# Performance work log

Measured on AMD Instinct MI355X. Metric: run time of the kernel, lower is better.

## Reference

```python
import jax, jax.numpy as jnp
import numpy as np
from jax import lax

H = 256       # hidden_size (hard-coded via .view(256,1) in source)
V = 10000     # vocab
NOPS = 9      # ops: 0 sum, 1 count, 2 diff, 3 greater, 4 lesser, 5 and, 6 or, 7 assign, 8 reset
COLS = 64
ROWS = 200000
T = 4         # num_time_steps
QLEN = 40
NNUM = 5


def setup_inputs() -> dict:
    key = jax.random.key(0)
    ks = jax.random.split(key, 16)
    s = 0.02
    return {
        'input_question': jax.random.randint(ks[0], (QLEN,), 0, V),
        'question_numbers': jax.random.normal(ks[1], (NNUM,), jnp.float32),
        'left_word_indices': jax.random.randint(ks[2], (NNUM,), 0, QLEN),
        'table': jax.random.normal(ks[3], (ROWS, COLS), jnp.float32),
        # question RNN params
        'E': jax.random.normal(ks[4], (V, H), jnp.float32) * s,
        'Wx': jax.random.normal(ks[5], (H, H), jnp.float32) * s,
        'Wh': jax.random.normal(ks[6], (H, H), jnp.float32) * s,
        'b': jnp.zeros((H,), jnp.float32),
        # selector params
        'W_op': jax.random.normal(ks[7], (H, 2 * H), jnp.float32) * s,
        'op_emb': jax.random.normal(ks[8], (NOPS, H), jnp.float32) * s,
        'W_col': jax.random.normal(ks[9], (H, 2 * H), jnp.float32) * s,
        'col_emb': jax.random.normal(ks[10], (COLS, H), jnp.float32) * s,
        # pivot embeddings U(0)=lesser, U(1)=greater
        'U': jax.random.normal(ks[11], (2, H), jnp.float32) * s,
        # history RNN params
        'W_hc': jax.random.normal(ks[12], (H, 2 * H), jnp.float32) * s,
        'W_hh': jax.random.normal(ks[13], (H, H), jnp.float32) * s,
    }


def reference(input_question, question_numbers, left_word_indices, table,
              E, Wx, Wh, b, W_op, op_emb, W_col, col_emb, U, W_hc, W_hh):
    rows = table.shape[0]
    # ---- question RNN (simple tanh RNN over embedded words) ----
    x = E[input_question]                                  # [Q, H]
    def cell(h, xt):
        hn = jnp.tanh(xt @ Wx + h @ Wh + b)
        return hn, hn
    q, states = lax.scan(cell, jnp.zeros((H,), table.dtype), x)   # q: [H], states: [Q, H]
    Z = states[left_word_indices]                          # z_matrix [N, H]

    # ---- pivots (train mode: soft attention over question numbers) ----
    beta_l = jax.nn.softmax(Z @ U[0])                      # [N]
    beta_g = jax.nn.softmax(Z @ U[1])
    l_pivot = beta_l @ question_numbers                    # scalar
    g_pivot = beta_g @ question_numbers

    row_selects = [jnp.ones((rows,), table.dtype)]
    scalars = [jnp.zeros((), table.dtype)]
    h_hist = jnp.zeros((H,), table.dtype)
    lookup = jnp.zeros(table.shape, table.dtype)

    for t in range(T):
        qh = jnp.concatenate([q, h_hist])                  # [2H]
        a_op = jax.nn.softmax(op_emb @ jnp.tanh(W_op @ qh))    # [NOPS]
        a_col = jax.nn.softmax(col_emb @ jnp.tanh(W_col @ qh)) # [COLS]

        rs1 = row_selects[-1]
        rs2 = row_selects[max(0, len(row_selects) - 2)]
        s1 = scalars[-1]
        s3 = scalars[max(0, len(scalars) - 3)]

        col_val = table @ a_col                            # [R] column-weighted table values
        g_sel = (table > g_pivot).astype(table.dtype) @ a_col  # [R]
        l_sel = (table < l_pivot).astype(table.dtype) @ a_col

        row_select = (a_op[3] * g_sel + a_op[4] * l_sel
                      + a_op[5] * jnp.minimum(rs1, rs2)
                      + a_op[6] * jnp.maximum(rs1, rs2)
                      + a_op[8] * 1.0
                      + (a_op[0] + a_op[1] + a_op[2] + a_op[7]) * rs1)

        scalar = (a_op[0] * (rs1 @ col_val)
                  + a_op[1] * jnp.sum(rs1)
                  + a_op[2] * (s3 - s1))

        lookup = a_op[7] * row_select[:, None] * a_col[None, :]   # [R, C]

        c = jnp.concatenate([a_op @ op_emb, a_col @ col_emb])     # [2H]
        h_hist = jnp.tanh(W_hc @ c + W_hh @ h_hist)

        row_selects.append(row_select)
        scalars.append(scalar)

    return scalars[-1], lookup
```

## Files before the change

kernel.cpp:

```cpp
#include <hip/hip_runtime.h>
#include <hip/hip_fp16.h>
#include <math.h>

#define H 256
#define COLSN 64
#define ROWSN 200000
#define T_STEPS 4
#define QLEN 40
#define NNUM 5
#define NOPS 9

#define WS_XWB    0
#define WS_Q      10240
#define WS_AOP    10496
#define WS_ACOL   10560
#define WS_PIV    10816
#define WS_TICKET 10818
#define WS_PACC8  10824
#define WS_MOP    11104
#define WS_MCOL   13408
#define WS_WPK    30720
#define WS_END    (30720 + 768*128 + 512*128)

#define NTBL_TILES  1563
#define NTBL_BLOCKS 782
#define NXW 10
#define NMB 72
#define NPK 20

template<int CTRL>
__device__ __forceinline__ float dpp_add(float x) {
    int xi = __float_as_int(x);
    int yi = __builtin_amdgcn_update_dpp(0, xi, CTRL, 0xF, 0xF, true);
    return x + __int_as_float(yi);
}
#define DPP_XOR1 0xB1
#define DPP_XOR2 0x4E
#define DPP_HMIR 0x141
#define DPP_MIR  0x140

__device__ __forceinline__ float reduce16(float v) {
    v = dpp_add<DPP_XOR1>(v);
    v = dpp_add<DPP_XOR2>(v);
    v = dpp_add<DPP_HMIR>(v);
    v = dpp_add<DPP_MIR>(v);
    return v;
}

__device__ __forceinline__ float fast_tanh(float x) {
    float cx = fminf(15.f, fmaxf(-15.f, x));
    float e = __expf(2.f * cx);
    return __fdividef(e - 1.f, e + 1.f);
}

__device__ __forceinline__ float dot4(float4 a, float4 b) {
    return a.x * b.x + a.y * b.y + a.z * b.z + a.w * b.w;
}

__device__ __forceinline__ int sw(int i) { return i + ((i >> 4) << 2); }

__device__ __forceinline__ const float* wrow_src(int o,
        const float* W_op, const float* W_col, const float* W_hh) {
    if (o < 256)  return &W_op[(long)o * 512 + 256];
    if (o < 512)  return &W_col[(long)(o - 256) * 512 + 256];
    if (o < 768)  return &W_hh[(long)(o - 512) * 256];
    if (o < 1024) return &W_op[(long)(o - 768) * 512];
    return &W_col[(long)(o - 1024) * 512];
}

__global__ __launch_bounds__(1024) void k_pre(const int* __restrict__ iq,
        const float* __restrict__ E, const float* __restrict__ Wx,
        const float* __restrict__ b, const float* __restrict__ W_hc,
        const float* __restrict__ op_emb, const float* __restrict__ col_emb,
        const float* __restrict__ W_op, const float* __restrict__ W_col,
        const float* __restrict__ W_hh, float* __restrict__ ws) {
    int blk = blockIdx.x;
    int tid = threadIdx.x;
    if (blk < NXW) {
        if (blk == 0 && tid < 16) ws[WS_TICKET + tid] = 0.f;
        int widx = blk * 4 + (tid >> 8);
        int i = tid & 255;
        int word = iq[widx];
        const float* erow = E + (long)word * H;
        float a0 = b[i], a1 = 0.f, a2 = 0.f, a3 = 0.f;
        #pragma unroll 8
        for (int j = 0; j < H; j += 4) {
            a0 += erow[j + 0] * Wx[(j + 0) * H + i];
            a1 += erow[j + 1] * Wx[(j + 1) * H + i];
            a2 += erow[j + 2] * Wx[(j + 2) * H + i];
            a3 += erow[j + 3] * Wx[(j + 3) * H + i];
        }
        ws[WS_XWB + widx * H + i] = (a0 + a1) + (a2 + a3);
    } else if (blk < NXW + NMB) {
        __shared__ __attribute__((aligned(16))) float tile[32][268];
        int mb = blk - NXW;
        int bi = mb / 9;
        int kg = mb % 9;
        int ibase = bi * 32;
        int coff = (kg == 0) ? 0 : H;
        for (int idx = tid; idx < 32 * 64; idx += 1024) {
            int rr = idx >> 6, c4 = idx & 63;
            float4 v = *(const float4*)&W_hc[(long)(ibase + rr) * 512 + coff + c4 * 4];
            float* d = &tile[rr][c4 * 4];
            d[0] = v.x; d[1] = v.y; d[2] = v.z; d[3] = v.w;
        }
        __syncthreads();
        int io = tid >> 5;
        int l32 = tid & 31;
        int nk = (kg == 0) ? NOPS : 8;
        for (int kk = 0; kk < nk; ++kk) {
            const float* emb;
            int dst;
            if (kg == 0) { emb = op_emb + kk * H; dst = WS_MOP + kk * H; }
            else { int c = (kg - 1) * 8 + kk; emb = col_emb + c * H; dst = WS_MCOL + c * H; }
            float s = 0.f;
            #pragma unroll
            for (int q8 = 0; q8 < 8; ++q8) {
                int q = (q8 + l32) & 7;
                s += tile[io][l32 * 8 + q] * emb[l32 * 8 + q];
            }
            s += __shfl_xor(s, 1);
            s += __shfl_xor(s, 2);
            s += __shfl_xor(s, 4);
            s += __shfl_xor(s, 8);
            s += __shfl_xor(s, 16);
            if (l32 == 0) ws[dst + ibase + io] = s;
        }
    } else {
        int pb2 = blk - NXW - NMB;
        int wb = pb2 * 64;
        __half2* wpk = (__half2*)(ws + WS_WPK);
        for (int idx = tid; idx < 64 * 128; idx += 1024) {
            int rr = idx >> 7, j2 = idx & 127;
            int o = wb + rr;
            const float* src = wrow_src(o, W_op, W_col, W_hh);
            float2 v = *(const float2*)&src[j2 * 2];
            wpk[(long)o * 128 + j2] = __floats2half2_rn(v.x, v.y);
        }
    }
}

__global__ __launch_bounds__(1024) void k_rnn(const float* __restrict__ Wh,
                      const int* __restrict__ lwi,
                      const float* __restrict__ U, const float* __restrict__ qn,
                      float* __restrict__ ws) {
    __shared__ __attribute__((aligned(16))) float hbuf[2][288];
    __shared__ __attribute__((aligned(16))) float xwb[QLEN][H];
    __shared__ float Z[NNUM][H];
    __shared__ float lg[10];
    int tid = threadIdx.x;
    int g = tid >> 3;
    int p = tid & 7;

    float2 w2[32];
    #pragma unroll
    for (int jj = 0; jj < 32; ++jj)
        w2[jj] = *(const float2*)&Wh[(p * 32 + jj) * H + g * 2];

    {
        const float4* src = (const float4*)&ws[WS_XWB];
        float4* dst = (float4*)&xwb[0][0];
        for (int idx = tid; idx < QLEN * H / 4; idx += 1024) dst[idx] = src[idx];
    }
    if (tid < H) hbuf[0][tid + ((tid >> 5) << 2)] = 0.f;
    __syncthreads();

    int lw0 = lwi[0], lw1 = lwi[1], lw2 = lwi[2], lw3 = lwi[3], lw4 = lwi[4];
    int cur = 0;
    for (int t = 0; t < QLEN; ++t) {
        const float4* hv = (const float4*)&hbuf[cur][p * 36];
        float a0 = 0.f, a1 = 0.f;
        #pragma unroll
        for (int q4 = 0; q4 < 8; ++q4) {
            float4 h4 = hv[q4];
            float2 wa = w2[q4 * 4 + 0];
            float2 wb = w2[q4 * 4 + 1];
            float2 wc = w2[q4 * 4 + 2];
            float2 wd = w2[q4 * 4 + 3];
            a0 += h4.x * wa.x; a1 += h4.x * wa.y;
            a0 += h4.y * wb.x; a1 += h4.y * wb.y;
            a0 += h4.z * wc.x; a1 += h4.z * wc.y;
            a0 += h4.w * wd.x; a1 += h4.w * wd.y;
        }
        a0 = dpp_add<DPP_XOR1>(a0); a0 = dpp_add<DPP_XOR2>(a0); a0 = dpp_add<DPP_HMIR>(a0);
        a1 = dpp_add<DPP_XOR1>(a1); a1 = dpp_add<DPP_XOR2>(a1); a1 = dpp_add<DPP_HMIR>(a1);
        if (p < 2) {
            float s = (p == 0) ? a0 : a1;
            int i = g * 2 + p;
            float hn = fast_tanh(xwb[t][i] + s);
            hbuf[cur ^ 1][i + ((i >> 5) << 2)] = hn;
            if (t == lw0) Z[0][i] = hn;
            if (t == lw1) Z[1][i] = hn;
            if (t == lw2) Z[2][i] = hn;
            if (t == lw3) Z[3][i] = hn;
            if (t == lw4) Z[4][i] = hn;
        }
        __syncthreads();
        cur ^= 1;
    }
    if (tid < H) ws[WS_Q + tid] = hbuf[cur][tid + ((tid >> 5) << 2)];

    int grp = tid >> 5;
    int lane = tid & 31;
    if (grp < 10) {
        int u = grp / 5, n = grp % 5;
        float s = 0.f;
        #pragma unroll
        for (int k = 0; k < 8; ++k) {
            int j = lane + k * 32;
            s += Z[n][j] * U[u * H + j];
        }
        s += __shfl_xor(s, 1);
        s += __shfl_xor(s, 2);
        s += __shfl_xor(s, 4);
        s += __shfl_xor(s, 8);
        s += __shfl_xor(s, 16);
        if (lane == 0) lg[grp] = s;
    }
    __syncthreads();
    if (tid < 2) {
        float m = -1e30f;
        for (int n = 0; n < 5; ++n) m = fmaxf(m, lg[tid * 5 + n]);
        float e[5], s = 0.f;
        for (int n = 0; n < 5; ++n) { e[n] = expf(lg[tid * 5 + n] - m); s += e[n]; }
        float piv = 0.f;
        for (int n = 0; n < 5; ++n) piv += (e[n] / s) * qn[n];
        ws[WS_PIV + (tid == 0 ? 1 : 0)] = piv;
    }
}

template<bool PACKED>
__device__ __forceinline__ void sel_body(
        const float* __restrict__ W_op, const float* __restrict__ W_col,
        const float* __restrict__ W_hh, const float* __restrict__ op_emb,
        const float* __restrict__ col_emb, float* __restrict__ ws) {
    __shared__ float mlds[73 * 256];
    __shared__ __attribute__((aligned(16))) float hl[320];
    __shared__ __attribute__((aligned(16))) float uop[320];
    __shared__ __attribute__((aligned(16))) float ucol[320];
    __shared__ float vhh[256];
    __shared__ float Pl[512];
    __shared__ float lgs[80];
    __shared__ float aop_s[16], acol_s[64];
    const int tid = threadIdx.x;
    const int r  = tid >> 4;
    const int p  = tid & 15;
    const int pb = p * 20;
    const __half2* wpk = (const __half2*)(ws + WS_WPK);

    for (int idx = tid; idx < 73 * 256; idx += 1024) mlds[idx] = ws[WS_MOP + idx];
    if (tid < 256) hl[sw(tid)] = ws[WS_Q + tid];
    __syncthreads();

    {
        float4 q0 = *(const float4*)&hl[pb + 0];
        float4 q1 = *(const float4*)&hl[pb + 4];
        float4 q2 = *(const float4*)&hl[pb + 8];
        float4 q3 = *(const float4*)&hl[pb + 12];
        float qv[16] = {q0.x,q0.y,q0.z,q0.w, q1.x,q1.y,q1.z,q1.w,
                        q2.x,q2.y,q2.z,q2.w, q3.x,q3.y,q3.z,q3.w};
        #pragma unroll 2
        for (int m = 0; m < 8; ++m) {
            int o = m * 64 + r;
            float s = 0.f;
            if (PACKED) {
                const __half2* row = wpk + (long)(768 + o) * 128 + p * 8;
                #pragma unroll
                for (int jj = 0; jj < 8; ++jj) {
                    float2 w = __half22float2(row[jj]);
                    s += w.x * qv[2 * jj] + w.y * qv[2 * jj + 1];
                }
            } else {
                const float* row = (o < 256) ? &W_op[(long)o * 512 + p * 16]
                                             : &W_col[(long)(o - 256) * 512 + p * 16];
                s = dot4(*(const float4*)&row[0], q0) + dot4(*(const float4*)&row[4], q1)
                  + dot4(*(const float4*)&row[8], q2) + dot4(*(const float4*)&row[12], q3);
            }
            s = reduce16(s);
            if (p == 0) Pl[o] = s;
        }
    }
    __syncthreads();
    if (tid < 256) {
        uop[sw(tid)]  = fast_tanh(Pl[tid]);
        ucol[sw(tid)] = fast_tanh(Pl[256 + tid]);
        vhh[tid] = 0.f;
    }
    __syncthreads();

    for (int t = 0; t < T_STEPS; ++t) {
        {
            const float* urow = &ucol[pb];
            float4 u0 = *(const float4*)&urow[0];
            float4 u1 = *(const float4*)&urow[4];
            float4 u2 = *(const float4*)&urow[8];
            float4 u3 = *(const float4*)&urow[12];
            const float* erow = &col_emb[r * 256 + p * 16];
            float s = dot4(*(const float4*)&erow[0], u0) + dot4(*(const float4*)&erow[4], u1)
                    + dot4(*(const float4*)&erow[8], u2) + dot4(*(const float4*)&erow[12], u3);
            s = reduce16(s);
            if (p == 0) lgs[NOPS + r] = s;
            if (r < NOPS) {
                const float* vrow = &uop[pb];
                float4 v0 = *(const float4*)&vrow[0];
                float4 v1 = *(const float4*)&vrow[4];
                float4 v2 = *(const float4*)&vrow[8];
                float4 v3 = *(const float4*)&vrow[12];
                const float* orow = &op_emb[r * 256 + p * 16];
                float so = dot4(*(const float4*)&orow[0], v0) + dot4(*(const float4*)&orow[4], v1)
                         + dot4(*(const float4*)&orow[8], v2) + dot4(*(const float4*)&orow[12], v3);
                so = reduce16(so);
                if (p == 0) lgs[r] = so;
            }
        }
        __syncthreads();
        if (tid == 0) {
            float m = -1e30f;
            for (int k = 0; k < NOPS; ++k) m = fmaxf(m, lgs[k]);
            float e[NOPS], s = 0.f;
            for (int k = 0; k < NOPS; ++k) { e[k] = expf(lgs[k] - m); s += e[k]; }
            float inv = 1.f / s;
            for (int k = 0; k < NOPS; ++k) {
                float a = e[k] * inv;
                aop_s[k] = a;
                ws[WS_AOP + t * 16 + k] = a;
            }
        }
        if (tid >= 64 && tid < 128) {
            int lane = tid - 64;
            float v = lgs[NOPS + lane];
            float m = v;
            for (int off = 1; off < 64; off <<= 1) m = fmaxf(m, __shfl_xor(m, off));
            float e = expf(v - m);
            float s = e;
            for (int off = 1; off < 64; off <<= 1) s += __shfl_xor(s, off);
            float a = __fdividef(e, s);
            acol_s[lane] = a;
            ws[WS_ACOL + t * COLSN + lane] = a;
        }
        __syncthreads();
        if (t < T_STEPS - 1) {
            if (tid < 256) {
                float s = vhh[tid];
                #pragma unroll
                for (int k = 0; k < NOPS; ++k) s += aop_s[k] * mlds[k * 256 + tid];
                #pragma unroll 8
                for (int c = 0; c < COLSN; ++c) s += acol_s[c] * mlds[(NOPS + c) * 256 + tid];
                hl[sw(tid)] = fast_tanh(s);
            }
            __syncthreads();
            {
                float4 h0 = *(const float4*)&hl[pb + 0];
                float4 h1 = *(const float4*)&hl[pb + 4];
                float4 h2 = *(const float4*)&hl[pb + 8];
                float4 h3 = *(const float4*)&hl[pb + 12];
                float hv2[16] = {h0.x,h0.y,h0.z,h0.w, h1.x,h1.y,h1.z,h1.w,
                                 h2.x,h2.y,h2.z,h2.w, h3.x,h3.y,h3.z,h3.w};
                #pragma unroll 2
                for (int m = 0; m < 12; ++m) {
                    int o = m * 64 + r;
                    float s = 0.f;
                    if (PACKED) {
                        const __half2* row = wpk + (long)o * 128 + p * 8;
                        #pragma unroll
                        for (int jj = 0; jj < 8; ++jj) {
                            float2 w = __half22float2(row[jj]);
                            s += w.x * hv2[2 * jj] + w.y * hv2[2 * jj + 1];
                        }
                    } else {
                        const float* row;
                        if (o < 256)      row = &W_op[(long)o * 512 + 256 + p * 16];
                        else if (o < 512) row = &W_col[(long)(o - 256) * 512 + 256 + p * 16];
                        else              row = &W_hh[(long)(o - 512) * 256 + p * 16];
                        s = dot4(*(const float4*)&row[0], h0) + dot4(*(const float4*)&row[4], h1)
                          + dot4(*(const float4*)&row[8], h2) + dot4(*(const float4*)&row[12], h3);
                    }
                    s = reduce16(s);
                    if (p == 0) {
                        if (o < 256)      uop[sw(o)] = fast_tanh(Pl[o] + s);
                        else if (o < 512) ucol[sw(o - 256)] = fast_tanh(Pl[o] + s);
                        else              vhh[o - 512] = s;
                    }
                }
            }
            __syncthreads();
        }
    }
}

__global__ __launch_bounds__(1024) void k_sel2_f16(
        const float* __restrict__ W_op, const float* __restrict__ W_col,
        const float* __restrict__ W_hh, const float* __restrict__ op_emb,
        const float* __restrict__ col_emb, float* __restrict__ ws) {
    sel_body<true>(W_op, W_col, W_hh, op_emb, col_emb, ws);
}
__global__ __launch_bounds__(1024) void k_sel2_f32(
        const float* __restrict__ W_op, const float* __restrict__ W_col,
        const float* __restrict__ W_hh, const float* __restrict__ op_emb,
        const float* __restrict__ col_emb, float* __restrict__ ws) {
    sel_body<false>(W_op, W_col, W_hh, op_emb, col_emb, ws);
}

__global__ __launch_bounds__(512) void k_table(const float* __restrict__ table,
                                               float* __restrict__ ws,
                                               float* __restrict__ out) {
    __shared__ __attribute__((aligned(16))) float4 acT4[4][17];
    __shared__ float aop_l[64];
    __shared__ float rs3s[8][16];
    __shared__ float bred[8][8];
    __shared__ int lastblk;
    const int tid = threadIdx.x;
    const int wid = tid >> 6;
    const int lane = tid & 63;
    const int r16 = lane & 15;
    const int q = lane >> 4;

    if (tid < 64) {
        aop_l[tid] = ws[WS_AOP + tid];
        acT4[tid >> 4][tid & 15] = make_float4(
            ws[WS_ACOL + 0 * COLSN + tid], ws[WS_ACOL + 1 * COLSN + tid],
            ws[WS_ACOL + 2 * COLSN + tid], ws[WS_ACOL + 3 * COLSN + tid]);
    }
    __syncthreads();
    const float gp = ws[WS_PIV + 0];
    const float lp = ws[WS_PIV + 1];
    const float ac3 = acT4[q][r16].w;

    long wrow0 = (long)blockIdx.x * 128 + wid * 16;
    long wrow1 = (long)(blockIdx.x + NTBL_BLOCKS) * 128 + wid * 16;
    bool act0 = wrow0 < ROWSN;
    bool act1 = wrow1 < ROWSN;

    float4 xa0, xa1, xa2, xa3, xb0, xb1, xb2, xb3;
    if (act0) {
        const float* src = table + (wrow0 + r16) * COLSN + q * 16;
        xa0 = *(const float4*)&src[0];
        xa1 = *(const float4*)&src[4];
        xa2 = *(const float4*)&src[8];
        xa3 = *(const float4*)&src[12];
    }
    if (act1) {
        const float* src = table + (wrow1 + r16) * COLSN + q * 16;
        xb0 = *(const float4*)&src[0];
        xb1 = *(const float4*)&src[4];
        xb2 = *(const float4*)&src[8];
        xb3 = *(const float4*)&src[12];
    }

    float dacc[4] = {0,0,0,0}, cacc[4] = {0,0,0,0};

    #define TBL_TILE(X0, X1, X2, X3, WROW, ACT)                                   \
    {                                                                             \
        float cv[4] = {0,0,0,0}, gs[4] = {0,0,0,0}, ls[4] = {0,0,0,0};            \
        if (ACT) {                                                                \
            float xs[16] = {X0.x,X0.y,X0.z,X0.w, X1.x,X1.y,X1.z,X1.w,             \
                            X2.x,X2.y,X2.z,X2.w, X3.x,X3.y,X3.z,X3.w};            \
            _Pragma("unroll")                                                     \
            for (int jj = 0; jj < 16; ++jj) {                                     \
                float x = xs[jj];                                                 \
                float4 a4 = acT4[q][jj];                                          \
                float gt = (x > gp) ? 1.f : 0.f;                                  \
                float lt = (x < lp) ? 1.f : 0.f;                                  \
                cv[0] += x * a4.x;  cv[1] += x * a4.y;                            \
                cv[2] += x * a4.z;  cv[3] += x * a4.w;                            \
                gs[0] += gt * a4.x; gs[1] += gt * a4.y;                           \
                gs[2] += gt * a4.z; gs[3] += gt * a4.w;                           \
                ls[0] += lt * a4.x; ls[1] += lt * a4.y;                           \
                ls[2] += lt * a4.z; ls[3] += lt * a4.w;                           \
            }                                                                     \
        }                                                                         \
        _Pragma("unroll")                                                         \
        for (int k = 0; k < 4; ++k) {                                             \
            cv[k] += __shfl_xor(cv[k], 16); cv[k] += __shfl_xor(cv[k], 32);       \
            gs[k] += __shfl_xor(gs[k], 16); gs[k] += __shfl_xor(gs[k], 32);       \
            ls[k] += __shfl_xor(ls[k], 16); ls[k] += __shfl_xor(ls[k], 32);       \
        }                                                                         \
        float prev1 = 1.f, prev2 = 1.f;                                           \
        _Pragma("unroll")                                                         \
        for (int t = 0; t < 4; ++t) {                                             \
            if (ACT) { dacc[t] += prev1 * cv[t]; cacc[t] += prev1; }              \
            float cg = aop_l[t*16+3], cl = aop_l[t*16+4], cmn = aop_l[t*16+5];    \
            float cmx = aop_l[t*16+6], co = aop_l[t*16+8];                        \
            float cid = aop_l[t*16+0] + aop_l[t*16+1]                             \
                      + aop_l[t*16+2] + aop_l[t*16+7];                            \
            float rsn = cg * gs[t] + cl * ls[t] + cmn * fminf(prev1, prev2)       \
                      + cmx * fmaxf(prev1, prev2) + co + cid * prev1;             \
            prev2 = prev1; prev1 = rsn;                                           \
        }                                                                         \
        if (q == 0 && ACT) rs3s[wid][r16] = prev1 * aop_l[3*16+7];                \
                        \
        if (ACT) {                                                                \
            float* dst = out + 1 + WROW * COLSN;                                  \
            _Pragma("unroll 4")                                                   \
            for (int s = 0; s < 16; ++s)                                          \
                __builtin_nontemporal_store(rs3s[wid][s] * ac3,                   \
                                            &dst[(long)s * COLSN + lane]);        \
        }                                                                         \
    }

    TBL_TILE(xa0, xa1, xa2, xa3, wrow0, act0)
    TBL_TILE(xb0, xb1, xb2, xb3, wrow1, act1)
    #undef TBL_TILE

    float vals[8];
    #pragma unroll
    for (int t = 0; t < 4; ++t) { vals[t] = dacc[t]; vals[4 + t] = cacc[t]; }
    #pragma unroll
    for (int k = 0; k < 8; ++k) vals[k] = reduce16(vals[k]);
    if (lane == 0) {
        #pragma unroll
        for (int k = 0; k < 8; ++k) bred[wid][k] = vals[k];
    }
    __syncthreads();
    if (tid < 8) {
        float s = 0.f;
        #pragma unroll
        for (int w = 0; w < 8; ++w) s += bred[w][tid];
        atomicAdd(&ws[WS_PACC8 + tid], s);
    }
    __syncthreads();

    if (tid == 0) {
        float old = atomicAdd(&ws[WS_TICKET], 1.0f);
        lastblk = ((int)(old + 0.5f) == NTBL_BLOCKS - 1) ? 1 : 0;
    }
    __syncthreads();
    if (lastblk) {
        if (tid < 8) bred[0][tid] = atomicAdd(&ws[WS_PACC8 + tid], 0.f);
        __syncthreads();
        if (tid == 0) {
            float d0 = bred[0][0], d1 = bred[0][1], d2 = bred[0][2], d3 = bred[0][3];
            float c0 = bred[0][4], c1 = bred[0][5], c2 = bred[0][6], c3 = bred[0][7];
            float s0 = aop_l[0]*d0  + aop_l[1]*c0;
            float s1 = aop_l[16]*d1 + aop_l[17]*c1 + aop_l[18]*(0.f - s0);
            float s2 = aop_l[32]*d2 + aop_l[33]*c2 + aop_l[34]*(0.f - s1);
            float s3 = aop_l[48]*d3 + aop_l[49]*c3 + aop_l[50]*(s0 - s2);
            out[0] = s3;
        }
    }
}

extern "C" void kernel_launch(void* const* d_in, const int* in_sizes, int n_in,
                              void* d_out, int out_size, void* d_ws, size_t ws_size,
                              hipStream_t stream) {
    const int*   iq      = (const int*)  d_in[0];
    const float* qn      = (const float*)d_in[1];
    const int*   lwi     = (const int*)  d_in[2];
    const float* table   = (const float*)d_in[3];
    const float* E       = (const float*)d_in[4];
    const float* Wx      = (const float*)d_in[5];
    const float* Wh      = (const float*)d_in[6];
    const float* b       = (const float*)d_in[7];
    const float* W_op    = (const float*)d_in[8];
    const float* op_emb  = (const float*)d_in[9];
    const float* W_col   = (const float*)d_in[10];
    const float* col_emb = (const float*)d_in[11];
    const float* U       = (const float*)d_in[12];
    const float* W_hc    = (const float*)d_in[13];
    const float* W_hh    = (const float*)d_in[14];
    float* out = (float*)d_out;
    float* ws  = (float*)d_ws;

    const bool packed = ws_size >= (size_t)WS_END * sizeof(float);
    int npre = NXW + NMB + (packed ? NPK : 0);

    hipLaunchKernelGGL(k_pre,  dim3(npre), dim3(1024), 0, stream,
                       iq, E, Wx, b, W_hc, op_emb, col_emb, W_op, W_col, W_hh, ws);
    hipLaunchKernelGGL(k_rnn,  dim3(1), dim3(1024), 0, stream, Wh, lwi, U, qn, ws);
    if (packed)
        hipLaunchKernelGGL(k_sel2_f16, dim3(1), dim3(1024), 0, stream,
                           W_op, W_col, W_hh, op_emb, col_emb, ws);
    else
        hipLaunchKernelGGL(k_sel2_f32, dim3(1), dim3(1024), 0, stream,
                           W_op, W_col, W_hh, op_emb, col_emb, ws);
    hipLaunchKernelGGL(k_table, dim3(NTBL_BLOCKS), dim3(512), 0, stream,
                       table, ws, out);
}
```

Before: 132.1 us.

## Prefetch table into cache with idle blocks during serial RNN and selector kernels

Launches the single-block RNN and selector kernels with 255 extra blocks that stream the whole 51 MB table and discard the values. The aim is to pull the table into the MI355X's on-chip cache (last-level cache) while the serial recurrent work runs, so the bandwidth-bound table kernel reads more of it from cache. The risk is that 51 MB may exceed the cache, and the extra blocks compete with the serial block for resources and bandwidth. The table is also read twice more from HBM in total.

```diff
diff --git a/kernel.cpp b/kernel.cpp
--- a/kernel.cpp
+++ b/kernel.cpp
@@ -27,6 +27,7 @@
 #define NXW 10
 #define NMB 72
 #define NPK 20
+#define NPF 255
 
 template<int CTRL>
 __device__ __forceinline__ float dpp_add(float x) {
@@ -58,6 +59,18 @@
 }
 
 __device__ __forceinline__ int sw(int i) { return i + ((i >> 4) << 2); }
+
+__device__ __forceinline__ void prefetch_table(const float* __restrict__ table,
+                                               int pfid, int tid) {
+    const float4* t4 = (const float4*)table;
+    const long n4 = (long)ROWSN * COLSN / 4;
+    float acc = 0.f;
+    for (long i = (long)pfid * 1024 + tid; i < n4; i += (long)NPF * 1024) {
+        float4 v = t4[i];
+        acc += v.x + v.y + v.z + v.w;
+    }
+    asm volatile("" :: "v"(acc));
+}
 
 __device__ __forceinline__ const float* wrow_src(int o,
         const float* W_op, const float* W_col, const float* W_hh) {
@@ -143,7 +156,11 @@
 __global__ __launch_bounds__(1024) void k_rnn(const float* __restrict__ Wh,
                       const int* __restrict__ lwi,
                       const float* __restrict__ U, const float* __restrict__ qn,
-                      float* __restrict__ ws) {
+                      const float* __restrict__ table, float* __restrict__ ws) {
+    if (blockIdx.x > 0) {
+        prefetch_table(table, blockIdx.x - 1, threadIdx.x);
+        return;
+    }
     __shared__ __attribute__((aligned(16))) float hbuf[2][288];
     __shared__ __attribute__((aligned(16))) float xwb[QLEN][H];
     __shared__ float Z[NNUM][H];
@@ -391,13 +408,17 @@
 __global__ __launch_bounds__(1024) void k_sel2_f16(
         const float* __restrict__ W_op, const float* __restrict__ W_col,
         const float* __restrict__ W_hh, const float* __restrict__ op_emb,
-        const float* __restrict__ col_emb, float* __restrict__ ws) {
+        const float* __restrict__ col_emb, const float* __restrict__ table,
+        float* __restrict__ ws) {
+    if (blockIdx.x > 0) { prefetch_table(table, blockIdx.x - 1, threadIdx.x); return; }
     sel_body<true>(W_op, W_col, W_hh, op_emb, col_emb, ws);
 }
 __global__ __launch_bounds__(1024) void k_sel2_f32(
         const float* __restrict__ W_op, const float* __restrict__ W_col,
         const float* __restrict__ W_hh, const float* __restrict__ op_emb,
-        const float* __restrict__ col_emb, float* __restrict__ ws) {
+        const float* __restrict__ col_emb, const float* __restrict__ table,
+        float* __restrict__ ws) {
+    if (blockIdx.x > 0) { prefetch_table(table, blockIdx.x - 1, threadIdx.x); return; }
     sel_body<false>(W_op, W_col, W_hh, op_emb, col_emb, ws);
 }
 
@@ -488,7 +509,6 @@
             prev2 = prev1; prev1 = rsn;                                           \
         }                                                                         \
         if (q == 0 && ACT) rs3s[wid][r16] = prev1 * aop_l[3*16+7];                \
-                        \
         if (ACT) {                                                                \
             float* dst = out + 1 + WROW * COLSN;                                  \
             _Pragma("unroll 4")                                                   \
@@ -566,13 +586,14 @@
 
     hipLaunchKernelGGL(k_pre,  dim3(npre), dim3(1024), 0, stream,
                        iq, E, Wx, b, W_hc, op_emb, col_emb, W_op, W_col, W_hh, ws);
-    hipLaunchKernelGGL(k_rnn,  dim3(1), dim3(1024), 0, stream, Wh, lwi, U, qn, ws);
+    hipLaunchKernelGGL(k_rnn,  dim3(1 + NPF), dim3(1024), 0, stream,
+                       Wh, lwi, U, qn, table, ws);
     if (packed)
-        hipLaunchKernelGGL(k_sel2_f16, dim3(1), dim3(1024), 0, stream,
-                           W_op, W_col, W_hh, op_emb, col_emb, ws);
+        hipLaunchKernelGGL(k_sel2_f16, dim3(1 + NPF), dim3(1024), 0, stream,
+                           W_op, W_col, W_hh, op_emb, col_emb, table, ws);
     else
-        hipLaunchKernelGGL(k_sel2_f32, dim3(1), dim3(1024), 0, stream,
-                           W_op, W_col, W_hh, op_emb, col_emb, ws);
+        hipLaunchKernelGGL(k_sel2_f32, dim3(1 + NPF), dim3(1024), 0, stream,
+                           W_op, W_col, W_hh, op_emb, col_emb, table, ws);
     hipLaunchKernelGGL(k_table, dim3(NTBL_BLOCKS), dim3(512), 0, stream,
                        table, ws, out);
 }
```

After: 137.5 us, median of 2. 1.04x slower.
